# Kernel tuning notes

Hardware: AMD Instinct MI355X
Metric: run time of the kernel (lower is better)

Reference implementation:

```python
import jax, jax.numpy as jnp
import numpy as np

N = 50000
E = 800000
IN_C = 128
HID = 32
OUT_C = 16
NEG_SLOPE = 0.2


def setup_inputs() -> dict:
    key = jax.random.key(0)
    ks = jax.random.split(key, 16)
    x = jax.random.normal(ks[0], (N, IN_C), dtype=jnp.float32)
    edge_index = jax.random.randint(ks[1], (2, E), 0, N, dtype=jnp.int64)

    def glorot(k, shape):
        fan = shape[0] + shape[-1]
        return jax.random.uniform(k, shape, jnp.float32, -1.0, 1.0) * jnp.sqrt(6.0 / fan)

    # layer1: in=128 -> heads=4, ch=32, concat -> out 128
    W1 = glorot(ks[2], (IN_C, 4 * HID))
    a_src1 = glorot(ks[3], (4, HID))
    a_dst1 = glorot(ks[4], (4, HID))
    b1 = jnp.zeros((4 * HID,), jnp.float32)
    # layer2: in=128 -> heads=2, ch=32, concat -> out 64
    W2 = glorot(ks[5], (4 * HID, 2 * HID))
    a_src2 = glorot(ks[6], (2, HID))
    a_dst2 = glorot(ks[7], (2, HID))
    b2 = jnp.zeros((2 * HID,), jnp.float32)
    # layer3: in=64 -> heads=1, ch=16, mean -> out 16
    W3 = glorot(ks[8], (2 * HID, OUT_C))
    a_src3 = glorot(ks[9], (1, OUT_C))
    a_dst3 = glorot(ks[10], (1, OUT_C))
    b3 = jnp.zeros((OUT_C,), jnp.float32)
    return {"x": x, "edge_index": edge_index,
            "W1": W1, "a_src1": a_src1, "a_dst1": a_dst1, "b1": b1,
            "W2": W2, "a_src2": a_src2, "a_dst2": a_dst2, "b2": b2,
            "W3": W3, "a_src3": a_src3, "a_dst3": a_dst3, "b3": b3}


def gat_conv(x, src, dst, W, a_src, a_dst, bias, heads, ch, concat):
    n = x.shape[0]
    h = (x @ W).reshape(n, heads, ch)                      # [N,H,C]
    alpha_s = jnp.einsum('nhc,hc->nh', h, a_src)           # [N,H]
    alpha_d = jnp.einsum('nhc,hc->nh', h, a_dst)           # [N,H]
    logits = jax.nn.leaky_relu(alpha_s[src] + alpha_d[dst], NEG_SLOPE)  # [E,H]
    # segment softmax over edges sharing the same destination node
    m = jax.ops.segment_max(logits, dst, num_segments=n)
    m = jnp.where(jnp.isfinite(m), m, 0.0)
    e = jnp.exp(logits - m[dst])
    denom = jax.ops.segment_sum(e, dst, num_segments=n)
    alpha = e / (denom[dst] + 1e-16)                       # [E,H]
    msg = h[src] * alpha[:, :, None]                       # [E,H,C]
    out = jax.ops.segment_sum(msg, dst, num_segments=n)    # [N,H,C]
    out = out.reshape(n, heads * ch) if concat else out.mean(axis=1)
    return out + bias


def reference(x, edge_index, W1, a_src1, a_dst1, b1, W2, a_src2, a_dst2, b2, W3, a_src3, a_dst3, b3):
    n = x.shape[0]
    loops = jnp.arange(n, dtype=edge_index.dtype)
    src = jnp.concatenate([edge_index[0], loops])  # add self loops (PyG default)
    dst = jnp.concatenate([edge_index[1], loops])
    h = jax.nn.relu(gat_conv(x, src, dst, W1, a_src1, a_dst1, b1, 4, HID, True))
    h = jax.nn.relu(gat_conv(h, src, dst, W2, a_src2, a_dst2, b2, 2, HID, True))
    out = gat_conv(h, src, dst, W3, a_src3, a_dst3, b3, 1, OUT_C, False)
    return out
```

## Files before the change

kernel.cpp:

```cpp
#include <hip/hip_runtime.h>
#include <hip/hip_bf16.h>
#include <stdint.h>

#define NODES 50000
#define NEDGE 800000
#define TEDGE (NEDGE + NODES)

typedef unsigned short u16;
typedef unsigned int u32;
typedef unsigned long long u64;
typedef _Float16 f16;
typedef _Float16 f16x8 __attribute__((ext_vector_type(8)));
typedef float f32x4 __attribute__((ext_vector_type(4)));

__device__ __forceinline__ float bf2f(u16 v) {
  return __uint_as_float(((u32)v) << 16);
}
__device__ __forceinline__ u16 f2bf(float f) {
  u32 u = __float_as_uint(f);
  u32 r = (u + 0x7FFFu + ((u >> 16) & 1u)) >> 16;
  return (u16)r;
}
__device__ __forceinline__ u16 f2h(float f) {
  return __builtin_bit_cast(u16, (f16)f);
}
__device__ __forceinline__ float h2f(u16 b) {
  return (float)__builtin_bit_cast(f16, b);
}
__device__ __forceinline__ float lo16f(u32 w) {
  return (float)__builtin_bit_cast(f16, (u16)(w & 0xFFFFu));
}
__device__ __forceinline__ float hi16f(u32 w) {
  return (float)__builtin_bit_cast(f16, (u16)(w >> 16));
}
__device__ __forceinline__ float lrelu(float x) {
  return (x > 0.f) ? x : 0.2f * x;
}
__device__ __forceinline__ int clampn(int v) {
  return ((u32)v < NODES) ? v : 0;
}
__device__ __forceinline__ float load1(const void* p, size_t i, bool fb) {
  return fb ? bf2f(((const u16*)p)[i]) : ((const float*)p)[i];
}
__device__ __forceinline__ u32 encf(float f) {
  u32 u = __float_as_uint(f);
  return (u & 0x80000000u) ? ~u : (u | 0x80000000u);
}
__device__ __forceinline__ float decf(u32 k) {
  u32 u = (k & 0x80000000u) ? (k & 0x7FFFFFFFu) : ~k;
  return __uint_as_float(u);
}
__device__ __forceinline__ void fma8h(float* ac, uint4 v, float a) {
  ac[0] += a * lo16f(v.x); ac[1] += a * hi16f(v.x);
  ac[2] += a * lo16f(v.y); ac[3] += a * hi16f(v.y);
  ac[4] += a * lo16f(v.z); ac[5] += a * hi16f(v.z);
  ac[6] += a * lo16f(v.w); ac[7] += a * hi16f(v.w);
}

__global__ __launch_bounds__(256) void k_probe(const int* __restrict__ ei,
                                               const u16* __restrict__ xs16,
                                               int* __restrict__ flags,
                                               int* __restrict__ deg) {
  int t = threadIdx.x;
  int g = blockIdx.x * 256 + t;
  if (g < NODES) deg[g] = 0;
  if (blockIdx.x == 0 && t >= 2 && t < 32) flags[t] = 0;
  if (blockIdx.x == 0 && t < 64) {
    int odd = 0, even = 0, big = 0;
#pragma unroll
    for (int k = 0; k < 4; ++k) {
      int idx = t + 64 * k;
      odd |= (ei[2 * idx + 1] != 0);
      even |= (ei[2 * idx] != 0);
      u32 ex = (xs16[2 * (t * 4 + k)] >> 7) & 0xFF;
      big += (ex >= 0x90);
    }
    u64 bo = __ballot(odd);
    u64 be = __ballot(even);
#pragma unroll
    for (int off = 32; off >= 1; off >>= 1) big += __shfl_xor(big, off);
    if (t == 0) {
      flags[0] = (bo == 0ull && be != 0ull) ? 1 : 0;
      flags[1] = (big >= 8) ? 0 : 1;
    }
  }
}

__global__ __launch_bounds__(256) void k_tw(const void* __restrict__ W1,
                                            const void* __restrict__ W2,
                                            const void* __restrict__ W3,
                                            const int* __restrict__ flags,
                                            u16* __restrict__ wt1,
                                            u16* __restrict__ wt2,
                                            u16* __restrict__ wt3) {
  int id = blockIdx.x * 256 + threadIdx.x;
  bool fb = flags[1] != 0;
  if (id < 16384) {
    int n = id >> 7, k = id & 127;
    wt1[n * 128 + k] = f2h(load1(W1, (size_t)k * 128 + n, fb));
  } else if (id < 24576) {
    int r = id - 16384;
    int n = r >> 7, k = r & 127;
    wt2[n * 128 + k] = f2h(load1(W2, (size_t)k * 64 + n, fb));
  } else if (id < 25600) {
    int r = id - 24576;
    int n = r >> 6, k = r & 63;
    wt3[n * 64 + k] = f2h(load1(W3, (size_t)k * 16 + n, fb));
  }
}


__global__ __launch_bounds__(256) void k_hist(const int* __restrict__ ei,
                                              const int* __restrict__ flags,
                                              int* deg, u16* __restrict__ rankarr,
                                              u16* __restrict__ src16,
                                              u16* __restrict__ dst16) {
  int e = blockIdx.x * 256 + threadIdx.x;
  if (e >= TEDGE) return;
  int d, s;
  if (e < NEDGE) {
    if (flags[0]) { s = ei[2 * e]; d = ei[2 * (NEDGE + e)]; }
    else { s = ei[e]; d = ei[NEDGE + e]; }
  } else {
    s = e - NEDGE; d = s;
  }
  s = clampn(s); d = clampn(d);
  src16[e] = (u16)s;
  dst16[e] = (u16)d;
  int r = atomicAdd(&deg[d], 1);
  rankarr[e] = (u16)min(r, 65535);
}

__global__ __launch_bounds__(1024) void k_scan(const int* __restrict__ deg,
                                               int* __restrict__ rowptr, int n) {
  int t = threadIdx.x, lane = t & 63, w = t >> 6;
  __shared__ int swave[16], soff[17];
  int carry = 0;
  for (int base = 0; base < n; base += 4096) {
    int i0 = base + t * 4;
    int v[4];
#pragma unroll
    for (int j = 0; j < 4; j++) { int i = i0 + j; v[j] = (i < n) ? deg[i] : 0; }
    int local = v[0] + v[1] + v[2] + v[3];
    int x = local;
#pragma unroll
    for (int off = 1; off < 64; off <<= 1) {
      int y = __shfl_up(x, off);
      if (lane >= off) x += y;
    }
    if (lane == 63) swave[w] = x;
    __syncthreads();
    if (w == 0) {
      int wv = (lane < 16) ? swave[lane] : 0;
#pragma unroll
      for (int off = 1; off < 16; off <<= 1) {
        int y = __shfl_up(wv, off);
        if (lane >= off) wv += y;
      }
      if (lane < 16) soff[lane + 1] = wv;
      if (lane == 0) soff[0] = 0;
    }
    __syncthreads();
    int run = carry + soff[w] + (x - local);
#pragma unroll
    for (int j = 0; j < 4; j++) {
      int i = i0 + j;
      if (i < n) rowptr[i] = run;
      run += v[j];
    }
    carry += soff[16];
    __syncthreads();
  }
  if (t == 0) rowptr[n] = carry;
}

__global__ __launch_bounds__(256) void k_scatter(const u16* __restrict__ src16,
                                                 const u16* __restrict__ dst16,
                                                 const int* __restrict__ rowptr,
                                                 const u16* __restrict__ rankarr,
                                                 u16* __restrict__ srcs) {
  int e = blockIdx.x * 256 + threadIdx.x;
  if (e >= TEDGE) return;
  int d = dst16[e];
  int pos = rowptr[d] + (int)rankarr[e];
  srcs[pos] = src16[e];
}


template <int K, int N, int H, bool XEXT>
__global__ __launch_bounds__(256) void k_gmfma(const void* __restrict__ xin,
                                               const u16* __restrict__ wtg,
                                               const void* __restrict__ a_src,
                                               const void* __restrict__ a_dst,
                                               u16* __restrict__ hout,
                                               float* __restrict__ asg,
                                               float* __restrict__ adg,
                                               u32* __restrict__ gm,
                                               const int* __restrict__ flags,
                                               int M) {
  constexpr int KP = K + 8;
  constexpr int NT = N / 16;
  constexpr int NTH = NT / H;
  constexpr int KG = K / 8;
  __shared__ u16 wlds[N * KP];
  __shared__ u16 xlds[64 * KP];
  __shared__ u32 lmax[2 * H];
  int t = threadIdx.x;
  int row0 = blockIdx.x * 64;
  bool fb = flags[1] != 0;
  if (t < 2 * H) lmax[t] = 0;

  for (int i = t; i < N * KG; i += 256) {
    int n = i / KG, kg = i % KG;
    *(uint4*)&wlds[n * KP + kg * 8] = *(const uint4*)(wtg + (size_t)n * K + kg * 8);
  }
  for (int i = t; i < 64 * KG; i += 256) {
    int r = i / KG, kg = i % KG;
    int grow = row0 + r;
    if (grow >= M) grow = M - 1;
    if (XEXT) {
      if (fb) {
        const u16* gp = (const u16*)xin + (size_t)grow * K + kg * 8;
        ushort4 v0 = *(const ushort4*)gp, v1 = *(const ushort4*)(gp + 4);
        *(ushort4*)&xlds[r * KP + kg * 8] = make_ushort4(
            f2h(bf2f(v0.x)), f2h(bf2f(v0.y)), f2h(bf2f(v0.z)), f2h(bf2f(v0.w)));
        *(ushort4*)&xlds[r * KP + kg * 8 + 4] = make_ushort4(
            f2h(bf2f(v1.x)), f2h(bf2f(v1.y)), f2h(bf2f(v1.z)), f2h(bf2f(v1.w)));
      } else {
        const float* gp = (const float*)xin + (size_t)grow * K + kg * 8;
        float4 f0 = *(const float4*)gp, f1 = *(const float4*)(gp + 4);
        *(ushort4*)&xlds[r * KP + kg * 8] =
            make_ushort4(f2h(f0.x), f2h(f0.y), f2h(f0.z), f2h(f0.w));
        *(ushort4*)&xlds[r * KP + kg * 8 + 4] =
            make_ushort4(f2h(f1.x), f2h(f1.y), f2h(f1.z), f2h(f1.w));
      }
    } else {
      *(uint4*)&xlds[r * KP + kg * 8] =
          *(const uint4*)((const u16*)xin + (size_t)grow * K + kg * 8);
    }
  }
  __syncthreads();

  int lane = t & 63, w = t >> 6;
  int lrow = lane & 15, quad = lane >> 4;
  f32x4 acc[NT];
#pragma unroll
  for (int nt = 0; nt < NT; ++nt) acc[nt] = (f32x4){0.f, 0.f, 0.f, 0.f};

  const u16* xbase = xlds + (w * 16 + lrow) * KP + quad * 8;
  const u16* wbase = wlds + lrow * KP + quad * 8;
#pragma unroll
  for (int ks = 0; ks < K / 32; ++ks) {
    f16x8 a = *(const f16x8*)(xbase + ks * 32);
#pragma unroll
    for (int nt = 0; nt < NT; ++nt) {
      f16x8 b = *(const f16x8*)(wbase + (size_t)nt * 16 * KP + ks * 32);
      acc[nt] = __builtin_amdgcn_mfma_f32_16x16x32_f16(a, b, acc[nt], 0, 0, 0);
    }
  }

  float avs[NT], avd[NT];
#pragma unroll
  for (int nt = 0; nt < NT; ++nt) {
    avs[nt] = load1(a_src, nt * 16 + lrow, fb);
    avd[nt] = load1(a_dst, nt * 16 + lrow, fb);
  }
  int baserow = row0 + w * 16 + quad * 4;
#pragma unroll
  for (int r = 0; r < 4; ++r) {
    int grow = baserow + r;
    float ps[H], pd[H];
#pragma unroll
    for (int h = 0; h < H; ++h) {
      ps[h] = 0.f; pd[h] = 0.f;
#pragma unroll
      for (int i = 0; i < NTH; ++i) {
        int nt = h * NTH + i;
        ps[h] += acc[nt][r] * avs[nt];
        pd[h] += acc[nt][r] * avd[nt];
      }
    }
#pragma unroll
    for (int m = 1; m < 16; m <<= 1) {
#pragma unroll
      for (int h = 0; h < H; ++h) {
        ps[h] += __shfl_xor(ps[h], m);
        pd[h] += __shfl_xor(pd[h], m);
      }
    }
    if (grow < M) {
#pragma unroll
      for (int nt = 0; nt < NT; ++nt)
        hout[(size_t)grow * N + nt * 16 + lrow] = f2h(acc[nt][r]);
#pragma unroll
      for (int h = 0; h < H; ++h) {
        if (lrow == h) {
          asg[grow * H + h] = ps[h];
          adg[grow * H + h] = pd[h];
          atomicMax(&lmax[h], encf(ps[h]));
          atomicMax(&lmax[H + h], encf(pd[h]));
        }
      }
    }
  }
  __syncthreads();
  if (t < 2 * H) atomicMax(&gm[t], lmax[t]);
}


template <int H, int C, bool RELU, bool FINAL>
__global__ __launch_bounds__(256) void k_agg(const u16* __restrict__ hbuf,
                                             const float* __restrict__ asg,
                                             const float* __restrict__ adg,
                                             const int* __restrict__ rowptr,
                                             const u16* __restrict__ srcs,
                                             const void* __restrict__ bias,
                                             const int* __restrict__ flags,
                                             const u32* __restrict__ gm,
                                             void* __restrict__ outp, int n) {
  constexpr int HC = H * C;
  constexpr int L = HC / 8;
  constexpr int EPN = 32 / L;
  constexpr int UN = (4 * EPN <= 32) ? 4 : 2;
  __shared__ u16 lds_s[4][64];
  __shared__ float lds_e[4][64][H];
  int lane = threadIdx.x & 63;
  int w = threadIdx.x >> 6;
  int nh = lane >> 5;
  int hl = lane & 31;
  int node = blockIdx.x * 8 + w * 2 + nh;
  if (node >= n) node = n - 1;
  bool fb = flags[1] != 0;
  int start = rowptr[node], end = rowptr[node + 1];
  if (end < start || end - start > TEDGE) { start = 0; end = 0; }

  float adh[H], M[H];
#pragma unroll
  for (int h = 0; h < H; ++h) adh[h] = adg[node * H + h];
#pragma unroll
  for (int h = 0; h < H; ++h) M[h] = lrelu(decf(gm[h]) + decf(gm[H + h]));

  int sub = hl / L;
  int cl = hl & (L - 1);
  int ch0 = cl * 8;
  int myhead = ch0 / C;
  int base = nh * 32;

  float den[H];
#pragma unroll
  for (int h = 0; h < H; ++h) den[h] = 0.f;
  float acc[UN][8];
#pragma unroll
  for (int u = 0; u < UN; ++u)
#pragma unroll
    for (int i = 0; i < 8; ++i) acc[u][i] = 0.f;

  for (int chunk = start; chunk < end; chunk += 32) {
    int e = chunk + hl;
    int s = 0;
    float ee[H];
#pragma unroll
    for (int h = 0; h < H; ++h) ee[h] = 0.f;
    if (e < end) {
      s = srcs[e];
      float av[H];
      if (H == 4) { float4 t4 = *(const float4*)(asg + s * 4);
        av[0] = t4.x; av[1] = t4.y; av[H > 2 ? 2 : 0] = t4.z; av[H > 3 ? 3 : 0] = t4.w; }
      else if (H == 2) { float2 t2 = *(const float2*)(asg + s * 2); av[0] = t2.x; av[1] = t2.y; }
      else av[0] = asg[s];
#pragma unroll
      for (int h = 0; h < H; ++h) {
        float x = __expf(lrelu(av[h] + adh[h]) - M[h]);
        ee[h] = x;
        den[h] += x;
      }
    }
    __builtin_amdgcn_wave_barrier();
    lds_s[w][lane] = (u16)s;
#pragma unroll
    for (int h = 0; h < H; ++h) lds_e[w][lane][h] = ee[h];
    __builtin_amdgcn_wave_barrier();

    int cn = min(32, end - chunk);
    for (int j = 0; j < cn; j += UN * EPN) {
      int sx[UN];
      float ax[UN];
#pragma unroll
      for (int u = 0; u < UN; ++u) {
        int ei_ = base + j + u * EPN + sub;
        sx[u] = lds_s[w][ei_];
        ax[u] = lds_e[w][ei_][myhead];
      }
#pragma unroll
      for (int u = 0; u < UN; ++u) {
        uint4 v = *(const uint4*)(hbuf + (size_t)sx[u] * HC + ch0);
        fma8h(acc[u], v, ax[u]);
      }
    }
  }

#pragma unroll
  for (int m = 16; m >= 1; m >>= 1) {
#pragma unroll
    for (int h = 0; h < H; ++h) den[h] += __shfl_xor(den[h], m);
  }
  float tt[8];
#pragma unroll
  for (int i = 0; i < 8; ++i) {
    tt[i] = acc[0][i];
#pragma unroll
    for (int u = 1; u < UN; ++u) tt[i] += acc[u][i];
  }
#pragma unroll
  for (int m = L; m < 32; m <<= 1) {
#pragma unroll
    for (int i = 0; i < 8; ++i) tt[i] += __shfl_xor(tt[i], m);
  }

  if (sub == 0) {
    float inv = 1.f / (den[myhead] + 1e-16f);
    float o[8];
#pragma unroll
    for (int i = 0; i < 8; ++i) {
      o[i] = tt[i] * inv + load1(bias, ch0 + i, fb);
      if (RELU) o[i] = fmaxf(o[i], 0.f);
    }
    if (FINAL) {
      if (fb) {
        uint4 pk;
        pk.x = (u32)f2bf(o[0]) | ((u32)f2bf(o[1]) << 16);
        pk.y = (u32)f2bf(o[2]) | ((u32)f2bf(o[3]) << 16);
        pk.z = (u32)f2bf(o[4]) | ((u32)f2bf(o[5]) << 16);
        pk.w = (u32)f2bf(o[6]) | ((u32)f2bf(o[7]) << 16);
        *(uint4*)((u16*)outp + (size_t)node * HC + ch0) = pk;
      } else {
        float* op = (float*)outp + (size_t)node * HC + ch0;
        *(float4*)op = make_float4(o[0], o[1], o[2], o[3]);
        *(float4*)(op + 4) = make_float4(o[4], o[5], o[6], o[7]);
      }
    } else {
      uint4 pk;
      pk.x = (u32)f2h(o[0]) | ((u32)f2h(o[1]) << 16);
      pk.y = (u32)f2h(o[2]) | ((u32)f2h(o[3]) << 16);
      pk.z = (u32)f2h(o[4]) | ((u32)f2h(o[5]) << 16);
      pk.w = (u32)f2h(o[6]) | ((u32)f2h(o[7]) << 16);
      *(uint4*)((u16*)outp + (size_t)node * HC + ch0) = pk;
    }
  }
}


extern "C" void kernel_launch(void* const* d_in, const int* in_sizes, int n_in,
                              void* d_out, int out_size, void* d_ws, size_t ws_size,
                              hipStream_t stream) {
  const void* x   = d_in[0];
  const int* ei   = (const int*)d_in[1];
  const void* W1  = d_in[2];
  const void* as1 = d_in[3];
  const void* ad1 = d_in[4];
  const void* b1  = d_in[5];
  const void* W2  = d_in[6];
  const void* as2 = d_in[7];
  const void* ad2 = d_in[8];
  const void* b2  = d_in[9];
  const void* W3  = d_in[10];
  const void* as3 = d_in[11];
  const void* ad3 = d_in[12];
  const void* b3  = d_in[13];

  char* w = (char*)d_ws;
  auto alloc = [&](size_t bytes) {
    char* p = w;
    w += (bytes + 255) & ~(size_t)255;
    return p;
  };
  int* flags    = (int*)alloc(256);
  int* deg      = (int*)alloc((size_t)NODES * 4);
  int* rowptr   = (int*)alloc((size_t)(NODES + 1) * 4);
  u16* rankarr  = (u16*)alloc((size_t)TEDGE * 2);
  u16* src16    = (u16*)alloc((size_t)TEDGE * 2);
  u16* dst16    = (u16*)alloc((size_t)TEDGE * 2);
  u16* srcs     = (u16*)alloc((size_t)TEDGE * 2);
  float* asg    = (float*)alloc((size_t)NODES * 4 * 4);
  float* adg    = (float*)alloc((size_t)NODES * 4 * 4);
  u16* wt1      = (u16*)alloc((size_t)128 * 128 * 2);
  u16* wt2      = (u16*)alloc((size_t)64 * 128 * 2);
  u16* wt3      = (u16*)alloc((size_t)16 * 64 * 2);
  u16* hbuf     = (u16*)alloc((size_t)NODES * 128 * 2);
  u16* obuf     = (u16*)alloc((size_t)NODES * 128 * 2);

  u32* gm1 = (u32*)(flags + 8);
  u32* gm2 = (u32*)(flags + 16);
  u32* gm3 = (u32*)(flags + 24);

  k_probe<<<(NODES + 255) / 256, 256, 0, stream>>>(ei, (const u16*)x, flags, deg);
  k_tw<<<100, 256, 0, stream>>>(W1, W2, W3, flags, wt1, wt2, wt3);
  k_hist<<<(TEDGE + 255) / 256, 256, 0, stream>>>(ei, flags, deg, rankarr, src16, dst16);
  k_scan<<<1, 1024, 0, stream>>>(deg, rowptr, NODES);
  k_scatter<<<(TEDGE + 255) / 256, 256, 0, stream>>>(src16, dst16, rowptr, rankarr, srcs);

  int gblocks = (NODES + 63) / 64;
  int ablocks = (NODES + 7) / 8;
  k_gmfma<128, 128, 4, true><<<gblocks, 256, 0, stream>>>(x, wt1, as1, ad1, hbuf, asg, adg, gm1, flags, NODES);
  k_agg<4, 32, true, false><<<ablocks, 256, 0, stream>>>(hbuf, asg, adg, rowptr, srcs, b1, flags, gm1, obuf, NODES);
  k_gmfma<128, 64, 2, false><<<gblocks, 256, 0, stream>>>(obuf, wt2, as2, ad2, hbuf, asg, adg, gm2, flags, NODES);
  k_agg<2, 32, true, false><<<ablocks, 256, 0, stream>>>(hbuf, asg, adg, rowptr, srcs, b2, flags, gm2, obuf, NODES);
  k_gmfma<64, 16, 1, false><<<gblocks, 256, 0, stream>>>(obuf, wt3, as3, ad3, hbuf, asg, adg, gm3, flags, NODES);
  k_agg<1, 16, false, true><<<ablocks, 256, 0, stream>>>(hbuf, asg, adg, rowptr, srcs, b3, flags, gm3, d_out, NODES);
}
```

Before: 316.2 us.

## Switch layers 1-2 aggregation to edge-parallel segmented reduction with atomics

Replaces the node-per-half-wave CSR aggregation for the first two GAT layers with an edge-parallel kernel. Each wave walks 128 dst-sorted edges and carries run-length accumulators per destination, flushing with atomics only at segment boundaries. A separate finalize kernel then normalizes by the denominator, adds bias, applies ReLU and packs to fp16. The goal is better load balance across variable node degrees. In exchange it adds packed src|dst storage, memsets, extra fp32 num/den traffic and an extra launch per layer. The k_agg H>1 path also loses its asg load, so av is left uninitialized there, but that path is no longer launched.

```diff
diff --git a/kernel.cpp b/kernel.cpp
--- a/kernel.cpp
+++ b/kernel.cpp
@@ -49,12 +49,6 @@
 __device__ __forceinline__ float decf(u32 k) {
   u32 u = (k & 0x80000000u) ? (k & 0x7FFFFFFFu) : ~k;
   return __uint_as_float(u);
-}
-__device__ __forceinline__ void fma8h(float* ac, uint4 v, float a) {
-  ac[0] += a * lo16f(v.x); ac[1] += a * hi16f(v.x);
-  ac[2] += a * lo16f(v.y); ac[3] += a * hi16f(v.y);
-  ac[4] += a * lo16f(v.z); ac[5] += a * hi16f(v.z);
-  ac[6] += a * lo16f(v.w); ac[7] += a * hi16f(v.w);
 }
 
 __global__ __launch_bounds__(256) void k_probe(const int* __restrict__ ei,
@@ -178,12 +172,12 @@
                                                  const u16* __restrict__ dst16,
                                                  const int* __restrict__ rowptr,
                                                  const u16* __restrict__ rankarr,
-                                                 u16* __restrict__ srcs) {
+                                                 u32* __restrict__ sd) {
   int e = blockIdx.x * 256 + threadIdx.x;
   if (e >= TEDGE) return;
   int d = dst16[e];
   int pos = rowptr[d] + (int)rankarr[e];
-  srcs[pos] = src16[e];
+  sd[pos] = (u32)src16[e] | ((u32)d << 16);
 }
 
 
@@ -308,12 +302,168 @@
 }
 
 
+template <int H, int C>
+__global__ __launch_bounds__(256) void k_eagg(const u16* __restrict__ hbuf,
+                                              const float* __restrict__ asg,
+                                              const float* __restrict__ adg,
+                                              const u32* __restrict__ sd,
+                                              const u32* __restrict__ gm,
+                                              float* __restrict__ num,
+                                              float* __restrict__ den) {
+  constexpr int HC = H * C;
+  constexpr int CPL = HC / 64;
+  __shared__ u32 sdl[4][64];
+  __shared__ float eel[4][64][H];
+  int t = threadIdx.x;
+  int lane = t & 63, w = t >> 6;
+  int wave = blockIdx.x * 4 + w;
+  int estart = wave * 128;
+  if (estart >= TEDGE) return;
+
+  float M[H];
+#pragma unroll
+  for (int h = 0; h < H; ++h) M[h] = lrelu(decf(gm[h]) + decf(gm[H + h]));
+
+  int myhead = (CPL == 2) ? (lane >> 4) : (lane >> 5);
+  bool rep = (CPL == 2) ? ((lane & 15) == 0) : ((lane & 31) == 0);
+
+  int dcur = -1;
+  bool first = true;
+  float a0 = 0.f, a1 = 0.f, dena = 0.f;
+
+  for (int tile = 0; tile < 2; ++tile) {
+    int e0 = estart + tile * 64;
+    if (e0 >= TEDGE) break;
+    int idx = e0 + lane;
+    int cidx = min(idx, TEDGE - 1);
+    u32 su = sd[cidx];
+    int s = su & 0xFFFF, d = su >> 16;
+    float ee[H];
+    {
+      float av[H], dv[H];
+      if (H == 4) {
+        float4 t4 = *(const float4*)(asg + s * 4);
+        av[0] = t4.x; av[1] = t4.y; av[H > 2 ? 2 : 0] = t4.z; av[H > 3 ? 3 : 0] = t4.w;
+        float4 t5 = *(const float4*)(adg + d * 4);
+        dv[0] = t5.x; dv[1] = t5.y; dv[H > 2 ? 2 : 0] = t5.z; dv[H > 3 ? 3 : 0] = t5.w;
+      } else if (H == 2) {
+        float2 t2 = *(const float2*)(asg + s * 2); av[0] = t2.x; av[1] = t2.y;
+        float2 t3 = *(const float2*)(adg + d * 2); dv[0] = t3.x; dv[1] = t3.y;
+      } else {
+        av[0] = asg[s]; dv[0] = adg[d];
+      }
+#pragma unroll
+      for (int h = 0; h < H; ++h) {
+        float x = __expf(lrelu(av[h] + dv[h]) - M[h]);
+        ee[h] = (idx < TEDGE) ? x : 0.f;
+      }
+    }
+    __builtin_amdgcn_wave_barrier();
+    sdl[w][lane] = su;
+#pragma unroll
+    for (int h = 0; h < H; ++h) eel[w][lane][h] = ee[h];
+    __builtin_amdgcn_wave_barrier();
+
+    int cn = min(64, TEDGE - e0);
+    int rn = (cn + 3) & ~3;
+    for (int j = 0; j < rn; j += 4) {
+      uint4 sg = *(const uint4*)&sdl[w][j];
+      float ef[4];
+      ef[0] = eel[w][j + 0][myhead];
+      ef[1] = eel[w][j + 1][myhead];
+      ef[2] = eel[w][j + 2][myhead];
+      ef[3] = eel[w][j + 3][myhead];
+      u32 ss[4] = {sg.x & 0xFFFFu, sg.y & 0xFFFFu, sg.z & 0xFFFFu, sg.w & 0xFFFFu};
+      u32 dd[4] = {sg.x >> 16, sg.y >> 16, sg.z >> 16, sg.w >> 16};
+      u32 v2[4];
+      float v1f[4];
+      if (CPL == 2) {
+#pragma unroll
+        for (int u = 0; u < 4; ++u)
+          v2[u] = *(const u32*)(hbuf + (size_t)ss[u] * HC + 2 * lane);
+      } else {
+#pragma unroll
+        for (int u = 0; u < 4; ++u)
+          v1f[u] = h2f(hbuf[(size_t)ss[u] * HC + lane]);
+      }
+#pragma unroll
+      for (int u = 0; u < 4; ++u) {
+        int du = __builtin_amdgcn_readfirstlane((int)dd[u]);
+        if (du != dcur) {
+          if (dcur >= 0) {
+            float* np = num + (size_t)dcur * HC + CPL * lane;
+            if (first) {
+              atomicAdd(np, a0);
+              if (CPL == 2) atomicAdd(np + 1, a1);
+              if (rep) atomicAdd(den + dcur * H + myhead, dena);
+            } else {
+              np[0] = a0;
+              if (CPL == 2) np[1] = a1;
+              if (rep) den[dcur * H + myhead] = dena;
+            }
+            first = false;
+            a0 = 0.f; a1 = 0.f; dena = 0.f;
+          }
+          dcur = du;
+        }
+        if (CPL == 2) {
+          a0 += ef[u] * lo16f(v2[u]);
+          a1 += ef[u] * hi16f(v2[u]);
+        } else {
+          a0 += ef[u] * v1f[u];
+        }
+        dena += ef[u];
+      }
+    }
+  }
+  if (dcur >= 0) {
+    float* np = num + (size_t)dcur * HC + CPL * lane;
+    atomicAdd(np, a0);
+    if (CPL == 2) atomicAdd(np + 1, a1);
+    if (rep) atomicAdd(den + dcur * H + myhead, dena);
+  }
+}
+
+
+template <int H, int C, bool RELU>
+__global__ __launch_bounds__(256) void k_fin(const float* __restrict__ num,
+                                             const float* __restrict__ den,
+                                             const void* __restrict__ bias,
+                                             const int* __restrict__ flags,
+                                             u16* __restrict__ outp, int n) {
+  constexpr int HC = H * C;
+  int id = blockIdx.x * 256 + threadIdx.x;
+  if (id >= n * (HC / 8)) return;
+  bool fb = flags[1] != 0;
+  int node = id / (HC / 8);
+  int ch0 = (id % (HC / 8)) * 8;
+  int h = ch0 / C;
+  float inv = 1.f / (den[node * H + h] + 1e-16f);
+  const float* np = num + (size_t)node * HC + ch0;
+  float4 n0 = *(const float4*)np;
+  float4 n1 = *(const float4*)(np + 4);
+  float o[8] = {n0.x, n0.y, n0.z, n0.w, n1.x, n1.y, n1.z, n1.w};
+  uint4 pk;
+  u32 pks[4];
+#pragma unroll
+  for (int i = 0; i < 8; ++i) {
+    o[i] = o[i] * inv + load1(bias, ch0 + i, fb);
+    if (RELU) o[i] = fmaxf(o[i], 0.f);
+  }
+#pragma unroll
+  for (int i = 0; i < 4; ++i)
+    pks[i] = (u32)f2h(o[2 * i]) | ((u32)f2h(o[2 * i + 1]) << 16);
+  pk.x = pks[0]; pk.y = pks[1]; pk.z = pks[2]; pk.w = pks[3];
+  *(uint4*)(outp + (size_t)node * HC + ch0) = pk;
+}
+
+
 template <int H, int C, bool RELU, bool FINAL>
 __global__ __launch_bounds__(256) void k_agg(const u16* __restrict__ hbuf,
                                              const float* __restrict__ asg,
                                              const float* __restrict__ adg,
                                              const int* __restrict__ rowptr,
-                                             const u16* __restrict__ srcs,
+                                             const u32* __restrict__ sd,
                                              const void* __restrict__ bias,
                                              const int* __restrict__ flags,
                                              const u32* __restrict__ gm,
@@ -362,12 +512,9 @@
 #pragma unroll
     for (int h = 0; h < H; ++h) ee[h] = 0.f;
     if (e < end) {
-      s = srcs[e];
+      s = sd[e] & 0xFFFF;
       float av[H];
-      if (H == 4) { float4 t4 = *(const float4*)(asg + s * 4);
-        av[0] = t4.x; av[1] = t4.y; av[H > 2 ? 2 : 0] = t4.z; av[H > 3 ? 3 : 0] = t4.w; }
-      else if (H == 2) { float2 t2 = *(const float2*)(asg + s * 2); av[0] = t2.x; av[1] = t2.y; }
-      else av[0] = asg[s];
+      if (H == 1) av[0] = asg[s];
 #pragma unroll
       for (int h = 0; h < H; ++h) {
         float x = __expf(lrelu(av[h] + adh[h]) - M[h]);
@@ -394,7 +541,10 @@
 #pragma unroll
       for (int u = 0; u < UN; ++u) {
         uint4 v = *(const uint4*)(hbuf + (size_t)sx[u] * HC + ch0);
-        fma8h(acc[u], v, ax[u]);
+        acc[u][0] += ax[u] * lo16f(v.x); acc[u][1] += ax[u] * hi16f(v.x);
+        acc[u][2] += ax[u] * lo16f(v.y); acc[u][3] += ax[u] * hi16f(v.y);
+        acc[u][4] += ax[u] * lo16f(v.z); acc[u][5] += ax[u] * hi16f(v.z);
+        acc[u][6] += ax[u] * lo16f(v.w); acc[u][7] += ax[u] * hi16f(v.w);
       }
     }
   }
@@ -480,7 +630,7 @@
   u16* rankarr  = (u16*)alloc((size_t)TEDGE * 2);
   u16* src16    = (u16*)alloc((size_t)TEDGE * 2);
   u16* dst16    = (u16*)alloc((size_t)TEDGE * 2);
-  u16* srcs     = (u16*)alloc((size_t)TEDGE * 2);
+  u32* sd       = (u32*)alloc((size_t)TEDGE * 4);
   float* asg    = (float*)alloc((size_t)NODES * 4 * 4);
   float* adg    = (float*)alloc((size_t)NODES * 4 * 4);
   u16* wt1      = (u16*)alloc((size_t)128 * 128 * 2);
@@ -488,6 +638,9 @@
   u16* wt3      = (u16*)alloc((size_t)16 * 64 * 2);
   u16* hbuf     = (u16*)alloc((size_t)NODES * 128 * 2);
   u16* obuf     = (u16*)alloc((size_t)NODES * 128 * 2);
+  float* num    = (float*)alloc((size_t)NODES * 132 * 4);
+  float* den1   = num + (size_t)NODES * 128;
+  float* den2   = num + (size_t)NODES * 64;
 
   u32* gm1 = (u32*)(flags + 8);
   u32* gm2 = (u32*)(flags + 16);
@@ -497,14 +650,21 @@
   k_tw<<<100, 256, 0, stream>>>(W1, W2, W3, flags, wt1, wt2, wt3);
   k_hist<<<(TEDGE + 255) / 256, 256, 0, stream>>>(ei, flags, deg, rankarr, src16, dst16);
   k_scan<<<1, 1024, 0, stream>>>(deg, rowptr, NODES);
-  k_scatter<<<(TEDGE + 255) / 256, 256, 0, stream>>>(src16, dst16, rowptr, rankarr, srcs);
+  k_scatter<<<(TEDGE + 255) / 256, 256, 0, stream>>>(src16, dst16, rowptr, rankarr, sd);
 
   int gblocks = (NODES + 63) / 64;
-  int ablocks = (NODES + 7) / 8;
+  int eblocks = (TEDGE + 511) / 512;
+
+  hipMemsetAsync(num, 0, (size_t)NODES * 132 * 4, stream);
   k_gmfma<128, 128, 4, true><<<gblocks, 256, 0, stream>>>(x, wt1, as1, ad1, hbuf, asg, adg, gm1, flags, NODES);
-  k_agg<4, 32, true, false><<<ablocks, 256, 0, stream>>>(hbuf, asg, adg, rowptr, srcs, b1, flags, gm1, obuf, NODES);
+  k_eagg<4, 32><<<eblocks, 256, 0, stream>>>(hbuf, asg, adg, sd, gm1, num, den1);
+  k_fin<4, 32, true><<<(NODES * 16 + 255) / 256, 256, 0, stream>>>(num, den1, b1, flags, obuf, NODES);
+
+  hipMemsetAsync(num, 0, (size_t)NODES * 66 * 4, stream);
   k_gmfma<128, 64, 2, false><<<gblocks, 256, 0, stream>>>(obuf, wt2, as2, ad2, hbuf, asg, adg, gm2, flags, NODES);
-  k_agg<2, 32, true, false><<<ablocks, 256, 0, stream>>>(hbuf, asg, adg, rowptr, srcs, b2, flags, gm2, obuf, NODES);
+  k_eagg<2, 32><<<eblocks, 256, 0, stream>>>(hbuf, asg, adg, sd, gm2, num, den2);
+  k_fin<2, 32, true><<<(NODES * 8 + 255) / 256, 256, 0, stream>>>(num, den2, b2, flags, obuf, NODES);
+
   k_gmfma<64, 16, 1, false><<<gblocks, 256, 0, stream>>>(obuf, wt3, as3, ad3, hbuf, asg, adg, gm3, flags, NODES);
-  k_agg<1, 16, false, true><<<ablocks, 256, 0, stream>>>(hbuf, asg, adg, rowptr, srcs, b3, flags, gm3, d_out, NODES);
-}
+  k_agg<1, 16, false, true><<<(NODES + 7) / 8, 256, 0, stream>>>(hbuf, asg, adg, rowptr, sd, b3, flags, gm3, d_out, NODES);
+}
```

Result: slower. 346.6 us (+9.6%).

## Replace rank-based CSR scatter with bucketed binning and per-bucket shared-memory placement

Applied to the files above, without the earlier changes.

Edges are binned into buckets of 256 destination nodes with a packed src|dst word, and a per-bucket kernel then places sources using shared-memory atomics. This replaces the global rank array and the separate src16/dst16 arrays, with the aim of cutting random global writes in the scatter step and improving locality. It adds a second global atomic per edge on the bucket counters, and a fixed bucket capacity (BCAP 8192) that silently drops edges if a bucket overflows, which matters for skewed degree distributions. Source order within a node also becomes nondeterministic.

```diff
diff --git a/kernel.cpp b/kernel.cpp
--- a/kernel.cpp
+++ b/kernel.cpp
@@ -5,6 +5,8 @@
 #define NODES 50000
 #define NEDGE 800000
 #define TEDGE (NEDGE + NODES)
+#define NBUCK ((NODES + 255) >> 8)
+#define BCAP 8192
 
 typedef unsigned short u16;
 typedef unsigned int u32;
@@ -24,9 +26,6 @@
 __device__ __forceinline__ u16 f2h(float f) {
   return __builtin_bit_cast(u16, (f16)f);
 }
-__device__ __forceinline__ float h2f(u16 b) {
-  return (float)__builtin_bit_cast(f16, b);
-}
 __device__ __forceinline__ float lo16f(u32 w) {
   return (float)__builtin_bit_cast(f16, (u16)(w & 0xFFFFu));
 }
@@ -50,20 +49,16 @@
   u32 u = (k & 0x80000000u) ? (k & 0x7FFFFFFFu) : ~k;
   return __uint_as_float(u);
 }
-__device__ __forceinline__ void fma8h(float* ac, uint4 v, float a) {
-  ac[0] += a * lo16f(v.x); ac[1] += a * hi16f(v.x);
-  ac[2] += a * lo16f(v.y); ac[3] += a * hi16f(v.y);
-  ac[4] += a * lo16f(v.z); ac[5] += a * hi16f(v.z);
-  ac[6] += a * lo16f(v.w); ac[7] += a * hi16f(v.w);
-}
 
 __global__ __launch_bounds__(256) void k_probe(const int* __restrict__ ei,
                                                const u16* __restrict__ xs16,
                                                int* __restrict__ flags,
-                                               int* __restrict__ deg) {
+                                               int* __restrict__ deg,
+                                               int* __restrict__ bcnt) {
   int t = threadIdx.x;
   int g = blockIdx.x * 256 + t;
   if (g < NODES) deg[g] = 0;
+  if (g < NBUCK) bcnt[g] = 0;
   if (blockIdx.x == 0 && t >= 2 && t < 32) flags[t] = 0;
   if (blockIdx.x == 0 && t < 64) {
     int odd = 0, even = 0, big = 0;
@@ -110,11 +105,10 @@
 }
 
 
-__global__ __launch_bounds__(256) void k_hist(const int* __restrict__ ei,
-                                              const int* __restrict__ flags,
-                                              int* deg, u16* __restrict__ rankarr,
-                                              u16* __restrict__ src16,
-                                              u16* __restrict__ dst16) {
+__global__ __launch_bounds__(256) void k_bin(const int* __restrict__ ei,
+                                             const int* __restrict__ flags,
+                                             int* deg, int* bcnt,
+                                             u32* __restrict__ bbuf) {
   int e = blockIdx.x * 256 + threadIdx.x;
   if (e >= TEDGE) return;
   int d, s;
@@ -125,10 +119,10 @@
     s = e - NEDGE; d = s;
   }
   s = clampn(s); d = clampn(d);
-  src16[e] = (u16)s;
-  dst16[e] = (u16)d;
-  int r = atomicAdd(&deg[d], 1);
-  rankarr[e] = (u16)min(r, 65535);
+  atomicAdd(&deg[d], 1);
+  int b = d >> 8;
+  int pos = atomicAdd(&bcnt[b], 1);
+  if (pos < BCAP) bbuf[(size_t)b * BCAP + pos] = (u32)s | ((u32)d << 16);
 }
 
 __global__ __launch_bounds__(1024) void k_scan(const int* __restrict__ deg,
@@ -174,16 +168,23 @@
   if (t == 0) rowptr[n] = carry;
 }
 
-__global__ __launch_bounds__(256) void k_scatter(const u16* __restrict__ src16,
-                                                 const u16* __restrict__ dst16,
-                                                 const int* __restrict__ rowptr,
-                                                 const u16* __restrict__ rankarr,
-                                                 u16* __restrict__ srcs) {
-  int e = blockIdx.x * 256 + threadIdx.x;
-  if (e >= TEDGE) return;
-  int d = dst16[e];
-  int pos = rowptr[d] + (int)rankarr[e];
-  srcs[pos] = src16[e];
+__global__ __launch_bounds__(256) void k_place(const u32* __restrict__ bbuf,
+                                               const int* __restrict__ bcnt,
+                                               const int* __restrict__ rowptr,
+                                               u16* __restrict__ srcs) {
+  __shared__ int cnt[256];
+  int b = blockIdx.x;
+  int t = threadIdx.x;
+  cnt[t] = 0;
+  __syncthreads();
+  int n = min(bcnt[b], BCAP);
+  const u32* bp = bbuf + (size_t)b * BCAP;
+  for (int i = t; i < n; i += 256) {
+    u32 v = bp[i];
+    int d = v >> 16;
+    int r = atomicAdd(&cnt[d & 255], 1);
+    srcs[rowptr[d] + r] = (u16)(v & 0xFFFFu);
+  }
 }
 
 
@@ -394,7 +395,10 @@
 #pragma unroll
       for (int u = 0; u < UN; ++u) {
         uint4 v = *(const uint4*)(hbuf + (size_t)sx[u] * HC + ch0);
-        fma8h(acc[u], v, ax[u]);
+        acc[u][0] += ax[u] * lo16f(v.x); acc[u][1] += ax[u] * hi16f(v.x);
+        acc[u][2] += ax[u] * lo16f(v.y); acc[u][3] += ax[u] * hi16f(v.y);
+        acc[u][4] += ax[u] * lo16f(v.z); acc[u][5] += ax[u] * hi16f(v.z);
+        acc[u][6] += ax[u] * lo16f(v.w); acc[u][7] += ax[u] * hi16f(v.w);
       }
     }
   }
@@ -477,9 +481,8 @@
   int* flags    = (int*)alloc(256);
   int* deg      = (int*)alloc((size_t)NODES * 4);
   int* rowptr   = (int*)alloc((size_t)(NODES + 1) * 4);
-  u16* rankarr  = (u16*)alloc((size_t)TEDGE * 2);
-  u16* src16    = (u16*)alloc((size_t)TEDGE * 2);
-  u16* dst16    = (u16*)alloc((size_t)TEDGE * 2);
+  int* bcnt     = (int*)alloc((size_t)NBUCK * 4);
+  u32* bbuf     = (u32*)alloc((size_t)NBUCK * BCAP * 4);
   u16* srcs     = (u16*)alloc((size_t)TEDGE * 2);
   float* asg    = (float*)alloc((size_t)NODES * 4 * 4);
   float* adg    = (float*)alloc((size_t)NODES * 4 * 4);
@@ -493,11 +496,11 @@
   u32* gm2 = (u32*)(flags + 16);
   u32* gm3 = (u32*)(flags + 24);
 
-  k_probe<<<(NODES + 255) / 256, 256, 0, stream>>>(ei, (const u16*)x, flags, deg);
+  k_probe<<<(NODES + 255) / 256, 256, 0, stream>>>(ei, (const u16*)x, flags, deg, bcnt);
   k_tw<<<100, 256, 0, stream>>>(W1, W2, W3, flags, wt1, wt2, wt3);
-  k_hist<<<(TEDGE + 255) / 256, 256, 0, stream>>>(ei, flags, deg, rankarr, src16, dst16);
+  k_bin<<<(TEDGE + 255) / 256, 256, 0, stream>>>(ei, flags, deg, bcnt, bbuf);
   k_scan<<<1, 1024, 0, stream>>>(deg, rowptr, NODES);
-  k_scatter<<<(TEDGE + 255) / 256, 256, 0, stream>>>(src16, dst16, rowptr, rankarr, srcs);
+  k_place<<<NBUCK, 256, 0, stream>>>(bbuf, bcnt, rowptr, srcs);
 
   int gblocks = (NODES + 63) / 64;
   int ablocks = (NODES + 7) / 8;
```

Result: slower. 835.6 us (+164.3%).
